# Kernel tuning notes

Hardware: AMD Instinct MI355X
Metric: run time of the kernel (lower is better)

The kernel has to match this reference:

```python
import jax, jax.numpy as jnp
import numpy as np

B, N, R, L = 32768, 9, 128, 2
F = 4 * R  # ffn hidden
EPS = 1e-5


def setup_inputs() -> dict:
    key = jax.random.key(0)
    ks = jax.random.split(key, 12)
    graph = jax.random.uniform(ks[0], (B, N, N), dtype=jnp.float32)  # weighted adjacency
    op_idx = jax.random.randint(ks[1], (B, N), 0, 7)
    op_table = jax.random.normal(ks[2], (7, R), dtype=jnp.float32)
    dev_embed = jax.random.normal(ks[3], (1, R), dtype=jnp.float32)
    s = 1.0 / np.sqrt(R)
    gcn_W = jax.random.normal(ks[4], (L, R, R), dtype=jnp.float32) * s
    gcn_b = jnp.zeros((L, R), dtype=jnp.float32)
    ln_g = jnp.ones((L, R), dtype=jnp.float32)
    ln_b = jnp.zeros((L, R), dtype=jnp.float32)
    ffn_W1 = jax.random.normal(ks[5], (L, R, F), dtype=jnp.float32) * s
    ffn_b1 = jnp.zeros((L, F), dtype=jnp.float32)
    ffn_W2 = jax.random.normal(ks[6], (L, F, R), dtype=jnp.float32) * (1.0 / np.sqrt(F))
    ffn_b2 = jnp.zeros((L, R), dtype=jnp.float32)
    fc_w = jax.random.normal(ks[7], (R, 1), dtype=jnp.float32) * s
    fc_b = jnp.zeros((1,), dtype=jnp.float32)
    return dict(graph=graph, op_idx=op_idx, op_table=op_table, dev_embed=dev_embed,
                gcn_W=gcn_W, gcn_b=gcn_b, ln_g=ln_g, ln_b=ln_b,
                ffn_W1=ffn_W1, ffn_b1=ffn_b1, ffn_W2=ffn_W2, ffn_b2=ffn_b2,
                fc_w=fc_w, fc_b=fc_b)


def _layer_norm(x, g, b):
    mu = x.mean(-1, keepdims=True)
    var = ((x - mu) ** 2).mean(-1, keepdims=True)
    return (x - mu) * jax.lax.rsqrt(var + EPS) * g + b


def reference(graph, op_idx, op_table, dev_embed, gcn_W, gcn_b, ln_g, ln_b,
              ffn_W1, ffn_b1, ffn_W2, ffn_b2, fc_w, fc_b):
    # embedding lookup + broadcast-add of device embedding: [B, N, R]
    x = op_table[op_idx].reshape(B * N, R) + dev_embed
    x = x.reshape(B, N, R)
    # symmetric GCN normalization with self loops on the 9x9 adjacency
    a_hat = graph + jnp.eye(N, dtype=graph.dtype)[None]
    d_is = jax.lax.rsqrt(a_hat.sum(-1))  # [B, N]
    norm_adj = a_hat * d_is[:, :, None] * d_is[:, None, :]  # [B, N, N]
    for l in range(L):
        # message passing + linear
        h = jnp.einsum('bij,bjr->bir', norm_adj, x) @ gcn_W[l] + gcn_b[l]
        h = jax.nn.relu(h)
        h = _layer_norm(h, ln_g[l], ln_b[l])
        # residual FFN
        h = h + jax.nn.relu(h @ ffn_W1[l] + ffn_b1[l]) @ ffn_W2[l] + ffn_b2[l]
        x = h
    pooled = x.mean(axis=1)  # [B, R] readout over the 9 nodes
    y = jax.nn.sigmoid(pooled @ fc_w + fc_b).squeeze(-1)  # [B]
    return y
```

## Files before the change

### kernel.cpp

```cpp
#include <hip/hip_runtime.h>
#include <math.h>

#define NN 9
#define RR 128
#define FF 512
#define LL 2
#define GPB 7
#define ROWS 63

typedef __attribute__((ext_vector_type(8))) short bf16x8;
typedef __attribute__((ext_vector_type(4))) float f32x4;

__device__ __forceinline__ float4 ld4(const float* p) { return *reinterpret_cast<const float4*>(p); }
__device__ __forceinline__ float2 ld2(const float* p) { return *reinterpret_cast<const float2*>(p); }
__device__ __forceinline__ void st4(float* p, const float4 v) { *reinterpret_cast<float4*>(p) = v; }

__device__ __forceinline__ ushort f2bf(float f) {
    unsigned u = __float_as_uint(f);
    return (ushort)((u + 0x7fffu + ((u >> 16) & 1u)) >> 16);
}
__device__ __forceinline__ float bf2f(ushort h) { return __uint_as_float(((unsigned)h) << 16); }

__device__ __forceinline__ void async16(void* lds, const void* g) {
    __builtin_amdgcn_global_load_lds(
        (const __attribute__((address_space(1))) unsigned int*)g,
        (__attribute__((address_space(3))) unsigned int*)lds,
        16, 0, 0);
}

#define SWZ(row, c) ((row) * 128 + ((c) ^ (((row) & 7) << 3)))

__global__ __launch_bounds__(256)
void pack_weights(const float* __restrict__ gcn_W,
                  const float* __restrict__ ffn_W1,
                  const float* __restrict__ ffn_W2,
                  ushort* __restrict__ wsw)
{
    const int t    = blockIdx.x * 256 + threadIdx.x;
    const int lane = t & 63;
    const int slot = t >> 6;
    const int grp  = lane >> 4, cl = lane & 15;

    const float* src; int ldn, kbase, n;
    if (slot < 64) {
        const int l = slot >> 5, ks = (slot >> 3) & 3, nt = slot & 7;
        src = gcn_W + l * RR * RR; ldn = RR;
        kbase = ks * 32 + grp * 8;
        n = nt * 16 + cl;
    } else if (slot < 320) {
        const int s = slot - 64;
        const int l = s >> 7, p = (s >> 5) & 3, ks = (s >> 3) & 3, nt = s & 7;
        src = ffn_W1 + l * RR * FF; ldn = FF;
        kbase = ks * 32 + grp * 8;
        n = p * 128 + nt * 16 + cl;
    } else {
        const int s = slot - 320;
        const int l = s >> 7, p = (s >> 5) & 3, ks = (s >> 3) & 3, nt = s & 7;
        src = ffn_W2 + l * FF * RR; ldn = RR;
        kbase = p * 128 + ks * 32 + grp * 8;
        n = nt * 16 + cl;
    }
    ushort v[8];
    #pragma unroll
    for (int j = 0; j < 8; ++j) v[j] = f2bf(src[(size_t)(kbase + j) * ldn + n]);
    uint4 o;
    o.x = v[0] | ((unsigned)v[1] << 16);
    o.y = v[2] | ((unsigned)v[3] << 16);
    o.z = v[4] | ((unsigned)v[5] << 16);
    o.w = v[6] | ((unsigned)v[7] << 16);
    *reinterpret_cast<uint4*>(wsw + ((size_t)slot * 64 + lane) * 8) = o;
}

__device__ __forceinline__ int g16(int l, int kh)         { return (l * 4 + kh * 2) * 8; }
__device__ __forceinline__ int w1g(int l, int p, int kh)  { return 64 + ((l * 4 + p) * 4 + kh * 2) * 8; }
__device__ __forceinline__ int w2g(int l, int p, int kh)  { return 320 + ((l * 4 + p) * 4 + kh * 2) * 8; }

#define MMA_GROUP2(T, APTR0, APTR1, BUFSEL)                                    \
    {                                                                          \
        const unsigned char* bb_ = &wbuf[BUFSEL][lane << 4];                   \
        const bf16x8 af0_ = *(const bf16x8*)(APTR0);                           \
        _Pragma("unroll")                                                      \
        for (int nt = 0; nt < 8; ++nt)                                         \
            T[nt] = __builtin_amdgcn_mfma_f32_16x16x32_bf16(                   \
                af0_, *(const bf16x8*)(bb_ + (nt << 10)), T[nt], 0, 0, 0);     \
        const bf16x8 af1_ = *(const bf16x8*)(APTR1);                           \
        _Pragma("unroll")                                                      \
        for (int nt = 0; nt < 8; ++nt)                                         \
            T[nt] = __builtin_amdgcn_mfma_f32_16x16x32_bf16(                   \
                af1_, *(const bf16x8*)(bb_ + ((8 + nt) << 10)), T[nt], 0, 0, 0); \
    }

#define STAGE16(DST, FRAGBASE)                                                 \
    {                                                                          \
        const unsigned char* g_ = wsb + ((size_t)((FRAGBASE) + ms * 4) << 10)  \
                                      + (lane << 4);                           \
        async16(&wbuf[DST][(ms * 4 + 0) << 10], g_);                           \
        async16(&wbuf[DST][(ms * 4 + 1) << 10], g_ + 1024);                    \
        async16(&wbuf[DST][(ms * 4 + 2) << 10], g_ + 2048);                    \
        async16(&wbuf[DST][(ms * 4 + 3) << 10], g_ + 3072);                    \
    }

__global__ __launch_bounds__(256, 2)
void backbone_mfma(const float* __restrict__ graph,
                   const int*   __restrict__ op_idx,
                   const float* __restrict__ op_table,
                   const float* __restrict__ dev_embed,
                   const float* __restrict__ gcn_b,
                   const float* __restrict__ ln_g,
                   const float* __restrict__ ln_b,
                   const float* __restrict__ ffn_b1,
                   const float* __restrict__ ffn_b2,
                   const float* __restrict__ fc_w,
                   const float* __restrict__ fc_b,
                   const ushort* __restrict__ wsw,
                   float* __restrict__ out,
                   const int nB)
{
    __shared__ alignas(16) ushort sA[64 * 128];
    __shared__ alignas(16) ushort sGH[64 * 128];
    __shared__ float sNA[GPB][81];
    __shared__ float sD[ROWS];
    __shared__ float sRD[64];
    __shared__ alignas(16) unsigned char wbuf[2][16384];

    const int tid  = threadIdx.x;
    const int lane = tid & 63;
    const int ms   = tid >> 6;
    const int grp  = lane >> 4;
    const int cl   = lane & 15;
    const int c0   = lane * 2;
    const int R0   = ms * 16;
    const int b0   = blockIdx.x * GPB;

    const unsigned char* wsb = (const unsigned char*)wsw;

    if (tid < 64) {
        *reinterpret_cast<unsigned*>(&sA[SWZ(63, tid * 2)])  = 0u;
        *reinterpret_cast<unsigned*>(&sGH[SWZ(63, tid * 2)]) = 0u;
    }

    {
        const float2 dv = ld2(&dev_embed[c0]);
        #pragma unroll
        for (int rr = 0; rr < 16; ++rr) {
            const int row = R0 + rr;
            if (row < ROWS) {
                const int gi = row / NN, ni = row - gi * NN;
                const int gg = min(b0 + gi, nB - 1);
                const int idx = op_idx[gg * NN + ni];
                float2 v = ld2(&op_table[idx * RR + c0]);
                unsigned pk = f2bf(v.x + dv.x) | ((unsigned)f2bf(v.y + dv.y) << 16);
                *reinterpret_cast<unsigned*>(&sA[SWZ(row, c0)]) = pk;
            }
        }
    }

    for (int e = tid; e < GPB * 81; e += 256) {
        const int gi = e / 81, r = e - gi * 81;
        const int i = r / NN, j = r - i * NN;
        const int gg = min(b0 + gi, nB - 1);
        sNA[gi][r] = graph[(size_t)gg * 81 + r] + (i == j ? 1.0f : 0.0f);
    }
    __syncthreads();
    if (tid < ROWS) {
        const int gi = tid / NN, i = tid - gi * NN;
        float s = 0.f;
        #pragma unroll
        for (int j = 0; j < NN; ++j) s += sNA[gi][i * NN + j];
        sD[tid] = rsqrtf(s);
    }
    __syncthreads();
    for (int e = tid; e < GPB * 81; e += 256) {
        const int gi = e / 81, r = e - gi * 81;
        const int i = r / NN, j = r - i * NN;
        sNA[gi][r] *= sD[gi * NN + i] * sD[gi * NN + j];
    }

    int cur = 0;
    STAGE16(0, g16(0, 0));
    __syncthreads();

    f32x4 acc[8];

    for (int l = 0; l < LL; ++l) {
        {
            const int g0 = R0 / NN, g1 = (R0 + 15) / NN;
            for (int gi = g0; gi <= g1 && gi < GPB; ++gi) {
                float xr[2 * NN];
                #pragma unroll
                for (int j = 0; j < NN; ++j) {
                    unsigned u = *reinterpret_cast<const unsigned*>(&sA[SWZ(gi * NN + j, c0)]);
                    xr[2 * j]     = bf2f((ushort)(u & 0xffffu));
                    xr[2 * j + 1] = bf2f((ushort)(u >> 16));
                }
                const int rlo = max(R0, gi * NN), rhi = min(R0 + 16, gi * NN + NN);
                for (int row = rlo; row < rhi; ++row) {
                    const int ni = row - gi * NN;
                    float a0 = 0.f, a1 = 0.f;
                    #pragma unroll
                    for (int j = 0; j < NN; ++j) {
                        const float w = sNA[gi][ni * NN + j];
                        a0 = fmaf(w, xr[2 * j], a0);
                        a1 = fmaf(w, xr[2 * j + 1], a1);
                    }
                    unsigned pk = f2bf(a0) | ((unsigned)f2bf(a1) << 16);
                    *reinterpret_cast<unsigned*>(&sGH[SWZ(row, c0)]) = pk;
                }
            }
        }

        #pragma unroll
        for (int nt = 0; nt < 8; ++nt) acc[nt] = (f32x4){0.f, 0.f, 0.f, 0.f};
        #pragma unroll
        for (int kh = 0; kh < 2; ++kh) {
            const int nb = (kh == 0) ? g16(l, 1) : w1g(l, 0, 0);
            STAGE16(cur ^ 1, nb);
            MMA_GROUP2(acc,
                       &sGH[SWZ(R0 + cl, (kh * 2 + 0) * 32 + grp * 8)],
                       &sGH[SWZ(R0 + cl, (kh * 2 + 1) * 32 + grp * 8)], cur);
            __syncthreads();
            cur ^= 1;
        }

        {
            float sv[4] = {0.f, 0.f, 0.f, 0.f}, qv[4] = {0.f, 0.f, 0.f, 0.f};
            #pragma unroll
            for (int nt = 0; nt < 8; ++nt) {
                const float gb = gcn_b[l * RR + nt * 16 + cl];
                #pragma unroll
                for (int r = 0; r < 4; ++r) {
                    float v = fmaxf(acc[nt][r] + gb, 0.f);
                    acc[nt][r] = v;
                    sv[r] += v; qv[r] += v * v;
                }
            }
            #pragma unroll
            for (int r = 0; r < 4; ++r) {
                #pragma unroll
                for (int m = 1; m <= 8; m <<= 1) {
                    sv[r] += __shfl_xor(sv[r], m);
                    qv[r] += __shfl_xor(qv[r], m);
                }
            }
            float mu[4], rs[4];
            #pragma unroll
            for (int r = 0; r < 4; ++r) {
                mu[r] = sv[r] * (1.f / RR);
                const float var = qv[r] * (1.f / RR) - mu[r] * mu[r];
                rs[r] = rsqrtf(var + 1e-5f);
            }
            #pragma unroll
            for (int nt = 0; nt < 8; ++nt) {
                const float lgv = ln_g[l * RR + nt * 16 + cl];
                const float lbv = ln_b[l * RR + nt * 16 + cl];
                #pragma unroll
                for (int r = 0; r < 4; ++r)
                    acc[nt][r] = (acc[nt][r] - mu[r]) * rs[r] * lgv + lbv;
            }
        }

        #pragma unroll
        for (int nt = 0; nt < 8; ++nt) {
            #pragma unroll
            for (int r = 0; r < 4; ++r)
                sA[SWZ(R0 + grp * 4 + r, nt * 16 + cl)] = f2bf(acc[nt][r]);
        }
        #pragma unroll
        for (int nt = 0; nt < 8; ++nt) {
            const float b2v = ffn_b2[l * RR + nt * 16 + cl];
            #pragma unroll
            for (int r = 0; r < 4; ++r) acc[nt][r] += b2v;
        }

        for (int p = 0; p < 4; ++p) {
            f32x4 t[8];
            #pragma unroll
            for (int nt = 0; nt < 8; ++nt) {
                const float b1v = ffn_b1[l * FF + p * 128 + nt * 16 + cl];
                t[nt] = (f32x4){b1v, b1v, b1v, b1v};
            }
            #pragma unroll
            for (int kh = 0; kh < 2; ++kh) {
                const int nb = (kh == 0) ? w1g(l, p, 1) : w2g(l, p, 0);
                STAGE16(cur ^ 1, nb);
                MMA_GROUP2(t,
                           &sA[SWZ(R0 + cl, (kh * 2 + 0) * 32 + grp * 8)],
                           &sA[SWZ(R0 + cl, (kh * 2 + 1) * 32 + grp * 8)], cur);
                __syncthreads();
                cur ^= 1;
            }
            #pragma unroll
            for (int nt = 0; nt < 8; ++nt) {
                #pragma unroll
                for (int r = 0; r < 4; ++r)
                    sGH[SWZ(R0 + grp * 4 + r, nt * 16 + cl)] = f2bf(fmaxf(t[nt][r], 0.f));
            }
            #pragma unroll
            for (int kh = 0; kh < 2; ++kh) {
                const bool last = (l == LL - 1) && (p == 3) && (kh == 1);
                const int nb = (kh == 0) ? w2g(l, p, 1)
                             : ((p < 3) ? w1g(l, p + 1, 0) : g16(l + 1, 0));
                if (!last) STAGE16(cur ^ 1, nb);
                MMA_GROUP2(acc,
                           &sGH[SWZ(R0 + cl, (kh * 2 + 0) * 32 + grp * 8)],
                           &sGH[SWZ(R0 + cl, (kh * 2 + 1) * 32 + grp * 8)], cur);
                __syncthreads();
                cur ^= 1;
            }
        }

        if (l + 1 < LL) {
            #pragma unroll
            for (int nt = 0; nt < 8; ++nt) {
                #pragma unroll
                for (int r = 0; r < 4; ++r)
                    sA[SWZ(R0 + grp * 4 + r, nt * 16 + cl)] = f2bf(acc[nt][r]);
            }
            __syncthreads();
        }
    }

    {
        float p4[4] = {0.f, 0.f, 0.f, 0.f};
        #pragma unroll
        for (int nt = 0; nt < 8; ++nt) {
            const float fw = fc_w[nt * 16 + cl];
            #pragma unroll
            for (int r = 0; r < 4; ++r) p4[r] = fmaf(acc[nt][r], fw, p4[r]);
        }
        #pragma unroll
        for (int r = 0; r < 4; ++r) {
            #pragma unroll
            for (int m = 1; m <= 8; m <<= 1) p4[r] += __shfl_xor(p4[r], m);
        }
        if (cl == 0) {
            #pragma unroll
            for (int r = 0; r < 4; ++r) sRD[R0 + grp * 4 + r] = p4[r];
        }
        __syncthreads();
        if (tid < GPB) {
            const int g = b0 + tid;
            if (g < nB) {
                float s = 0.f;
                #pragma unroll
                for (int n = 0; n < NN; ++n) s += sRD[tid * NN + n];
                out[g] = 1.f / (1.f + expf(-(s * (1.f / 9.f) + fc_b[0])));
            }
        }
    }
}

__device__ __forceinline__ void fma4(float4& d, const float a, const float4 w) {
    d.x = fmaf(a, w.x, d.x); d.y = fmaf(a, w.y, d.y);
    d.z = fmaf(a, w.z, d.z); d.w = fmaf(a, w.w, d.w);
}
__device__ __forceinline__ void xadd32(float4& v) {
    v.x += __shfl_xor(v.x, 32); v.y += __shfl_xor(v.y, 32);
    v.z += __shfl_xor(v.z, 32); v.w += __shfl_xor(v.w, 32);
}
__device__ __forceinline__ void relu4f(float4& v) {
    v.x = fmaxf(v.x, 0.f); v.y = fmaxf(v.y, 0.f);
    v.z = fmaxf(v.z, 0.f); v.w = fmaxf(v.w, 0.f);
}

__global__ __launch_bounds__(256)
void backbone_fp32(const float* __restrict__ graph, const int* __restrict__ op_idx,
                   const float* __restrict__ op_table, const float* __restrict__ dev_embed,
                   const float* __restrict__ gcn_W, const float* __restrict__ gcn_b,
                   const float* __restrict__ ln_g, const float* __restrict__ ln_b,
                   const float* __restrict__ ffn_W1, const float* __restrict__ ffn_b1,
                   const float* __restrict__ ffn_W2, const float* __restrict__ ffn_b2,
                   const float* __restrict__ fc_w, const float* __restrict__ fc_b,
                   float* __restrict__ out)
{
    __shared__ float sX[4][NN][RR];
    __shared__ float sT[4][NN][RR];
    __shared__ float sNA[4][81];
    __shared__ float sD[4][NN];

    const int tid  = threadIdx.x;
    const int lane = tid & 63;
    const int cg   = tid & 31;
    const int half = (tid >> 5) & 1;
    const int ms   = tid >> 6;
    const int c0   = cg * 4;
    const int k0   = half * 64;
    const int g    = blockIdx.x * 4 + ms;

    {
        const float dv0 = dev_embed[lane];
        const float dv1 = dev_embed[lane + 64];
        #pragma unroll
        for (int j = 0; j < NN; ++j) {
            const int idx = op_idx[g * NN + j];
            sX[ms][j][lane]      = op_table[idx * RR + lane]      + dv0;
            sX[ms][j][lane + 64] = op_table[idx * RR + lane + 64] + dv1;
        }
    }
    {
        const float* gp = graph + (size_t)g * 81;
        { const int i = lane / NN, j = lane - i * NN;
          sNA[ms][lane] = gp[lane] + (i == j ? 1.0f : 0.0f); }
        if (lane < 17) { const int e = lane + 64; const int i = e / NN, j = e - i * NN;
          sNA[ms][e] = gp[e] + (i == j ? 1.0f : 0.0f); }
        if (lane < NN) {
            float s = 0.f;
            #pragma unroll
            for (int j = 0; j < NN; ++j) s += sNA[ms][lane * NN + j];
            sD[ms][lane] = rsqrtf(s);
        }
        { const int i = lane / NN, j = lane - i * NN; sNA[ms][lane] *= sD[ms][i] * sD[ms][j]; }
        if (lane < 17) { const int e = lane + 64; const int i = e / NN, j = e - i * NN;
          sNA[ms][e] *= sD[ms][i] * sD[ms][j]; }
    }

    float4 acc[NN];
    for (int l = 0; l < LL; ++l) {
        const float* gw = gcn_W  + l * RR * RR;
        const float* gb = gcn_b  + l * RR;
        const float* lg = ln_g   + l * RR;
        const float* lb = ln_b   + l * RR;
        const float* w1 = ffn_W1 + l * RR * FF;
        const float* b1 = ffn_b1 + l * FF;
        const float* w2 = ffn_W2 + l * FF * RR;
        const float* b2 = ffn_b2 + l * RR;
        {
            float4 xv[NN];
            #pragma unroll
            for (int j = 0; j < NN; ++j) xv[j] = ld4(&sX[ms][j][c0]);
            #pragma unroll
            for (int ii = 0; ii < 5; ++ii) {
                const int i = ii + half * 5;
                if (i < NN) {
                    float4 a = make_float4(0.f, 0.f, 0.f, 0.f);
                    #pragma unroll
                    for (int j = 0; j < NN; ++j) fma4(a, sNA[ms][i * NN + j], xv[j]);
                    st4(&sT[ms][i][c0], a);
                }
            }
        }
        float4 h[NN];
        {
            const float4 z4 = make_float4(0.f, 0.f, 0.f, 0.f);
            const float4 gbv = ld4(&gb[c0]);
            const float4 ini = half ? z4 : gbv;
            #pragma unroll
            for (int i = 0; i < NN; ++i) h[i] = ini;
            #pragma unroll 2
            for (int kk = 0; kk < 64; kk += 4) {
                const float* wp = gw + (size_t)(k0 + kk) * RR + c0;
                const float4 wv0 = ld4(wp), wv1 = ld4(wp + RR), wv2 = ld4(wp + 2 * RR), wv3 = ld4(wp + 3 * RR);
                #pragma unroll
                for (int i = 0; i < NN; ++i) {
                    const float4 a = ld4(&sT[ms][i][k0 + kk]);
                    fma4(h[i], a.x, wv0); fma4(h[i], a.y, wv1);
                    fma4(h[i], a.z, wv2); fma4(h[i], a.w, wv3);
                }
            }
            #pragma unroll
            for (int i = 0; i < NN; ++i) xadd32(h[i]);
        }
        {
            const float4 lgv = ld4(&lg[c0]);
            const float4 lbv = ld4(&lb[c0]);
            #pragma unroll
            for (int i = 0; i < NN; ++i) {
                float4 v = h[i]; relu4f(v);
                float s = v.x + v.y + v.z + v.w;
                float q = v.x*v.x + v.y*v.y + v.z*v.z + v.w*v.w;
                #pragma unroll
                for (int m = 1; m <= 16; m <<= 1) { s += __shfl_xor(s, m); q += __shfl_xor(q, m); }
                const float mu = s * (1.f / RR);
                const float var = q * (1.f / RR) - mu * mu;
                const float rs = rsqrtf(var + 1e-5f);
                v.x = (v.x - mu) * rs * lgv.x + lbv.x;
                v.y = (v.y - mu) * rs * lgv.y + lbv.y;
                v.z = (v.z - mu) * rs * lgv.z + lbv.z;
                v.w = (v.w - mu) * rs * lgv.w + lbv.w;
                h[i] = v;
            }
        }
        #pragma unroll
        for (int i = 0; i < NN; ++i) st4(&sX[ms][i][c0], h[i]);
        {
            const float4 b2v = ld4(&b2[c0]);
            #pragma unroll
            for (int i = 0; i < NN; ++i) {
                if (half) acc[i] = make_float4(0.f, 0.f, 0.f, 0.f);
                else { acc[i] = h[i];
                       acc[i].x += b2v.x; acc[i].y += b2v.y; acc[i].z += b2v.z; acc[i].w += b2v.w; }
            }
        }
        for (int p = 0; p < 4; ++p) {
            const int f0 = p * RR + c0;
            float4 t[NN];
            {
                const float4 z4 = make_float4(0.f, 0.f, 0.f, 0.f);
                const float4 b1v = ld4(&b1[f0]);
                const float4 ini = half ? z4 : b1v;
                #pragma unroll
                for (int i = 0; i < NN; ++i) t[i] = ini;
            }
            #pragma unroll 2
            for (int kk = 0; kk < 64; kk += 4) {
                const float* wp = w1 + (size_t)(k0 + kk) * FF + f0;
                const float4 wv0 = ld4(wp), wv1 = ld4(wp + FF), wv2 = ld4(wp + 2 * FF), wv3 = ld4(wp + 3 * FF);
                #pragma unroll
                for (int i = 0; i < NN; ++i) {
                    const float4 a = ld4(&sX[ms][i][k0 + kk]);
                    fma4(t[i], a.x, wv0); fma4(t[i], a.y, wv1);
                    fma4(t[i], a.z, wv2); fma4(t[i], a.w, wv3);
                }
            }
            #pragma unroll
            for (int i = 0; i < NN; ++i) { xadd32(t[i]); relu4f(t[i]); st4(&sT[ms][i][c0], t[i]); }
            #pragma unroll 2
            for (int kk = 0; kk < 64; kk += 4) {
                const float* wp = w2 + (size_t)(p * RR + k0 + kk) * RR + c0;
                const float4 wv0 = ld4(wp), wv1 = ld4(wp + RR), wv2 = ld4(wp + 2 * RR), wv3 = ld4(wp + 3 * RR);
                #pragma unroll
                for (int i = 0; i < NN; ++i) {
                    const float4 a = ld4(&sT[ms][i][k0 + kk]);
                    fma4(acc[i], a.x, wv0); fma4(acc[i], a.y, wv1);
                    fma4(acc[i], a.z, wv2); fma4(acc[i], a.w, wv3);
                }
            }
        }
        #pragma unroll
        for (int i = 0; i < NN; ++i) xadd32(acc[i]);
        if (l + 1 < LL) {
            #pragma unroll
            for (int i = 0; i < NN; ++i) st4(&sX[ms][i][c0], acc[i]);
        }
    }
    {
        const float4 fw = ld4(&fc_w[c0]);
        float4 pv = make_float4(0.f, 0.f, 0.f, 0.f);
        #pragma unroll
        for (int i = 0; i < NN; ++i) { pv.x += acc[i].x; pv.y += acc[i].y; pv.z += acc[i].z; pv.w += acc[i].w; }
        float part = (pv.x*fw.x + pv.y*fw.y + pv.z*fw.z + pv.w*fw.w) * (1.f / 9.f);
        #pragma unroll
        for (int m = 1; m <= 16; m <<= 1) part += __shfl_xor(part, m);
        if (lane == 0) out[g] = 1.f / (1.f + expf(-(part + fc_b[0])));
    }
}

extern "C" void kernel_launch(void* const* d_in, const int* in_sizes, int n_in,
                              void* d_out, int out_size, void* d_ws, size_t ws_size,
                              hipStream_t stream) {
    const float* graph     = (const float*)d_in[0];
    const int*   op_idx    = (const int*)  d_in[1];
    const float* op_table  = (const float*)d_in[2];
    const float* dev_embed = (const float*)d_in[3];
    const float* gcn_W     = (const float*)d_in[4];
    const float* gcn_b     = (const float*)d_in[5];
    const float* ln_g      = (const float*)d_in[6];
    const float* ln_b      = (const float*)d_in[7];
    const float* ffn_W1    = (const float*)d_in[8];
    const float* ffn_b1    = (const float*)d_in[9];
    const float* ffn_W2    = (const float*)d_in[10];
    const float* ffn_b2    = (const float*)d_in[11];
    const float* fc_w      = (const float*)d_in[12];
    const float* fc_b      = (const float*)d_in[13];
    float* out = (float*)d_out;

    const int nB = in_sizes[0] / 81;
    const size_t WS_NEED = 576 * 1024;

    if (d_ws != nullptr && ws_size >= WS_NEED) {
        pack_weights<<<dim3(144), dim3(256), 0, stream>>>(gcn_W, ffn_W1, ffn_W2, (ushort*)d_ws);
        backbone_mfma<<<dim3((nB + GPB - 1) / GPB), dim3(256), 0, stream>>>(
            graph, op_idx, op_table, dev_embed, gcn_b, ln_g, ln_b,
            ffn_b1, ffn_b2, fc_w, fc_b, (const ushort*)d_ws, out, nB);
    } else {
        backbone_fp32<<<dim3(nB / 4), dim3(256), 0, stream>>>(
            graph, op_idx, op_table, dev_embed, gcn_W, gcn_b, ln_g, ln_b,
            ffn_W1, ffn_b1, ffn_W2, ffn_b2, fc_w, fc_b, out);
    }
}
```

Before: 384.7 us.

## Retile MFMA work per wave into 32-row by 64-column blocks

Result: no change. 389.7 us (+1.3%).

```diff
diff --git a/kernel.cpp b/kernel.cpp
--- a/kernel.cpp
+++ b/kernel.cpp
@@ -75,19 +75,23 @@
 __device__ __forceinline__ int w1g(int l, int p, int kh)  { return 64 + ((l * 4 + p) * 4 + kh * 2) * 8; }
 __device__ __forceinline__ int w2g(int l, int p, int kh)  { return 320 + ((l * 4 + p) * 4 + kh * 2) * 8; }
 
-#define MMA_GROUP2(T, APTR0, APTR1, BUFSEL)                                    \
+#define MMA22(T, SRCARR, KH, BUFSEL)                                           \
     {                                                                          \
         const unsigned char* bb_ = &wbuf[BUFSEL][lane << 4];                   \
-        const bf16x8 af0_ = *(const bf16x8*)(APTR0);                           \
         _Pragma("unroll")                                                      \
-        for (int nt = 0; nt < 8; ++nt)                                         \
-            T[nt] = __builtin_amdgcn_mfma_f32_16x16x32_bf16(                   \
-                af0_, *(const bf16x8*)(bb_ + (nt << 10)), T[nt], 0, 0, 0);     \
-        const bf16x8 af1_ = *(const bf16x8*)(APTR1);                           \
-        _Pragma("unroll")                                                      \
-        for (int nt = 0; nt < 8; ++nt)                                         \
-            T[nt] = __builtin_amdgcn_mfma_f32_16x16x32_bf16(                   \
-                af1_, *(const bf16x8*)(bb_ + ((8 + nt) << 10)), T[nt], 0, 0, 0); \
+        for (int ki = 0; ki < 2; ++ki) {                                       \
+            const bf16x8 a0_ = *(const bf16x8*)&SRCARR[SWZ(rh32 + cl,          \
+                                        ((KH) * 2 + ki) * 32 + grp * 8)];      \
+            const bf16x8 a1_ = *(const bf16x8*)&SRCARR[SWZ(rh32 + 16 + cl,     \
+                                        ((KH) * 2 + ki) * 32 + grp * 8)];      \
+            _Pragma("unroll")                                                  \
+            for (int nt = 0; nt < 4; ++nt) {                                   \
+                const bf16x8 b_ = *(const bf16x8*)(bb_ +                       \
+                                        ((ki * 8 + ch4 + nt) << 10));          \
+                T[nt]     = __builtin_amdgcn_mfma_f32_16x16x32_bf16(a0_, b_, T[nt], 0, 0, 0);     \
+                T[4 + nt] = __builtin_amdgcn_mfma_f32_16x16x32_bf16(a1_, b_, T[4 + nt], 0, 0, 0); \
+            }                                                                  \
+        }                                                                      \
     }
 
 #define STAGE16(DST, FRAGBASE)                                                 \
@@ -120,7 +124,8 @@
     __shared__ alignas(16) ushort sGH[64 * 128];
     __shared__ float sNA[GPB][81];
     __shared__ float sD[ROWS];
-    __shared__ float sRD[64];
+    __shared__ float2 sLN[64][2];
+    __shared__ float sRD[64][2];
     __shared__ alignas(16) unsigned char wbuf[2][16384];
 
     const int tid  = threadIdx.x;
@@ -129,6 +134,9 @@
     const int grp  = lane >> 4;
     const int cl   = lane & 15;
     const int c0   = lane * 2;
+    const int rh32 = (ms >> 1) * 32;
+    const int ch4  = (ms & 1) * 4;
+    const int cb   = ch4 * 16;
     const int R0   = ms * 16;
     const int b0   = blockIdx.x * GPB;
 
@@ -208,102 +216,129 @@
                 }
             }
         }
-
-        #pragma unroll
-        for (int nt = 0; nt < 8; ++nt) acc[nt] = (f32x4){0.f, 0.f, 0.f, 0.f};
+        __syncthreads();
+
+        #pragma unroll
+        for (int i = 0; i < 8; ++i) acc[i] = (f32x4){0.f, 0.f, 0.f, 0.f};
         #pragma unroll
         for (int kh = 0; kh < 2; ++kh) {
             const int nb = (kh == 0) ? g16(l, 1) : w1g(l, 0, 0);
             STAGE16(cur ^ 1, nb);
-            MMA_GROUP2(acc,
-                       &sGH[SWZ(R0 + cl, (kh * 2 + 0) * 32 + grp * 8)],
-                       &sGH[SWZ(R0 + cl, (kh * 2 + 1) * 32 + grp * 8)], cur);
+            MMA22(acc, sGH, kh, cur);
             __syncthreads();
             cur ^= 1;
         }
 
         {
-            float sv[4] = {0.f, 0.f, 0.f, 0.f}, qv[4] = {0.f, 0.f, 0.f, 0.f};
-            #pragma unroll
-            for (int nt = 0; nt < 8; ++nt) {
-                const float gb = gcn_b[l * RR + nt * 16 + cl];
+            float sv[8] = {0,0,0,0,0,0,0,0}, qv[8] = {0,0,0,0,0,0,0,0};
+            #pragma unroll
+            for (int rg = 0; rg < 2; ++rg) {
+                #pragma unroll
+                for (int nt = 0; nt < 4; ++nt) {
+                    const float gb = gcn_b[l * RR + cb + nt * 16 + cl];
+                    #pragma unroll
+                    for (int r = 0; r < 4; ++r) {
+                        float v = fmaxf(acc[rg * 4 + nt][r] + gb, 0.f);
+                        acc[rg * 4 + nt][r] = v;
+                        sv[rg * 4 + r] += v; qv[rg * 4 + r] += v * v;
+                    }
+                }
+            }
+            #pragma unroll
+            for (int i = 0; i < 8; ++i) {
+                #pragma unroll
+                for (int m = 1; m <= 8; m <<= 1) {
+                    sv[i] += __shfl_xor(sv[i], m);
+                    qv[i] += __shfl_xor(qv[i], m);
+                }
+            }
+            if (cl == 0) {
+                #pragma unroll
+                for (int rg = 0; rg < 2; ++rg)
+                    #pragma unroll
+                    for (int r = 0; r < 4; ++r)
+                        sLN[rh32 + rg * 16 + grp * 4 + r][ms & 1] =
+                            make_float2(sv[rg * 4 + r], qv[rg * 4 + r]);
+            }
+            __syncthreads();
+            float mu[8], rs[8];
+            #pragma unroll
+            for (int rg = 0; rg < 2; ++rg) {
                 #pragma unroll
                 for (int r = 0; r < 4; ++r) {
-                    float v = fmaxf(acc[nt][r] + gb, 0.f);
-                    acc[nt][r] = v;
-                    sv[r] += v; qv[r] += v * v;
-                }
-            }
-            #pragma unroll
-            for (int r = 0; r < 4; ++r) {
-                #pragma unroll
-                for (int m = 1; m <= 8; m <<= 1) {
-                    sv[r] += __shfl_xor(sv[r], m);
-                    qv[r] += __shfl_xor(qv[r], m);
-                }
-            }
-            float mu[4], rs[4];
-            #pragma unroll
-            for (int r = 0; r < 4; ++r) {
-                mu[r] = sv[r] * (1.f / RR);
-                const float var = qv[r] * (1.f / RR) - mu[r] * mu[r];
-                rs[r] = rsqrtf(var + 1e-5f);
-            }
-            #pragma unroll
-            for (int nt = 0; nt < 8; ++nt) {
-                const float lgv = ln_g[l * RR + nt * 16 + cl];
-                const float lbv = ln_b[l * RR + nt * 16 + cl];
+                    const float2 a = sLN[rh32 + rg * 16 + grp * 4 + r][0];
+                    const float2 b = sLN[rh32 + rg * 16 + grp * 4 + r][1];
+                    const float s = a.x + b.x, q = a.y + b.y;
+                    const float m_ = s * (1.f / RR);
+                    mu[rg * 4 + r] = m_;
+                    rs[rg * 4 + r] = rsqrtf(q * (1.f / RR) - m_ * m_ + 1e-5f);
+                }
+            }
+            #pragma unroll
+            for (int rg = 0; rg < 2; ++rg) {
+                #pragma unroll
+                for (int nt = 0; nt < 4; ++nt) {
+                    const float lgv = ln_g[l * RR + cb + nt * 16 + cl];
+                    const float lbv = ln_b[l * RR + cb + nt * 16 + cl];
+                    #pragma unroll
+                    for (int r = 0; r < 4; ++r)
+                        acc[rg * 4 + nt][r] = (acc[rg * 4 + nt][r] - mu[rg * 4 + r])
+                                              * rs[rg * 4 + r] * lgv + lbv;
+                }
+            }
+        }
+
+        #pragma unroll
+        for (int rg = 0; rg < 2; ++rg)
+            #pragma unroll
+            for (int nt = 0; nt < 4; ++nt)
                 #pragma unroll
                 for (int r = 0; r < 4; ++r)
-                    acc[nt][r] = (acc[nt][r] - mu[r]) * rs[r] * lgv + lbv;
-            }
-        }
-
-        #pragma unroll
-        for (int nt = 0; nt < 8; ++nt) {
-            #pragma unroll
-            for (int r = 0; r < 4; ++r)
-                sA[SWZ(R0 + grp * 4 + r, nt * 16 + cl)] = f2bf(acc[nt][r]);
-        }
-        #pragma unroll
-        for (int nt = 0; nt < 8; ++nt) {
-            const float b2v = ffn_b2[l * RR + nt * 16 + cl];
-            #pragma unroll
-            for (int r = 0; r < 4; ++r) acc[nt][r] += b2v;
-        }
+                    sA[SWZ(rh32 + rg * 16 + grp * 4 + r, cb + nt * 16 + cl)]
+                        = f2bf(acc[rg * 4 + nt][r]);
+        #pragma unroll
+        for (int rg = 0; rg < 2; ++rg)
+            #pragma unroll
+            for (int nt = 0; nt < 4; ++nt) {
+                const float b2v = ffn_b2[l * RR + cb + nt * 16 + cl];
+                #pragma unroll
+                for (int r = 0; r < 4; ++r) acc[rg * 4 + nt][r] += b2v;
+            }
+        __syncthreads();
 
         for (int p = 0; p < 4; ++p) {
             f32x4 t[8];
             #pragma unroll
-            for (int nt = 0; nt < 8; ++nt) {
-                const float b1v = ffn_b1[l * FF + p * 128 + nt * 16 + cl];
-                t[nt] = (f32x4){b1v, b1v, b1v, b1v};
-            }
+            for (int rg = 0; rg < 2; ++rg)
+                #pragma unroll
+                for (int nt = 0; nt < 4; ++nt) {
+                    const float b1v = ffn_b1[l * FF + p * 128 + cb + nt * 16 + cl];
+                    t[rg * 4 + nt] = (f32x4){b1v, b1v, b1v, b1v};
+                }
             #pragma unroll
             for (int kh = 0; kh < 2; ++kh) {
                 const int nb = (kh == 0) ? w1g(l, p, 1) : w2g(l, p, 0);
                 STAGE16(cur ^ 1, nb);
-                MMA_GROUP2(t,
-                           &sA[SWZ(R0 + cl, (kh * 2 + 0) * 32 + grp * 8)],
-                           &sA[SWZ(R0 + cl, (kh * 2 + 1) * 32 + grp * 8)], cur);
+                MMA22(t, sA, kh, cur);
                 __syncthreads();
                 cur ^= 1;
             }
             #pragma unroll
-            for (int nt = 0; nt < 8; ++nt) {
-                #pragma unroll
-                for (int r = 0; r < 4; ++r)
-                    sGH[SWZ(R0 + grp * 4 + r, nt * 16 + cl)] = f2bf(fmaxf(t[nt][r], 0.f));
-            }
+            for (int rg = 0; rg < 2; ++rg)
+                #pragma unroll
+                for (int nt = 0; nt < 4; ++nt)
+                    #pragma unroll
+                    for (int r = 0; r < 4; ++r)
+                        sGH[SWZ(rh32 + rg * 16 + grp * 4 + r, cb + nt * 16 + cl)]
+                            = f2bf(fmaxf(t[rg * 4 + nt][r], 0.f));
+            __syncthreads();
             #pragma unroll
             for (int kh = 0; kh < 2; ++kh) {
                 const bool last = (l == LL - 1) && (p == 3) && (kh == 1);
                 const int nb = (kh == 0) ? w2g(l, p, 1)
                              : ((p < 3) ? w1g(l, p + 1, 0) : g16(l + 1, 0));
                 if (!last) STAGE16(cur ^ 1, nb);
-                MMA_GROUP2(acc,
-                           &sGH[SWZ(R0 + cl, (kh * 2 + 0) * 32 + grp * 8)],
-                           &sGH[SWZ(R0 + cl, (kh * 2 + 1) * 32 + grp * 8)], cur);
+                MMA22(acc, sGH, kh, cur);
                 __syncthreads();
                 cur ^= 1;
             }
@@ -311,31 +346,39 @@
 
         if (l + 1 < LL) {
             #pragma unroll
-            for (int nt = 0; nt < 8; ++nt) {
+            for (int rg = 0; rg < 2; ++rg)
+                #pragma unroll
+                for (int nt = 0; nt < 4; ++nt)
+                    #pragma unroll
+                    for (int r = 0; r < 4; ++r)
+                        sA[SWZ(rh32 + rg * 16 + grp * 4 + r, cb + nt * 16 + cl)]
+                            = f2bf(acc[rg * 4 + nt][r]);
+            __syncthreads();
+        }
+    }
+
+    {
+        float p4[8] = {0,0,0,0,0,0,0,0};
+        #pragma unroll
+        for (int rg = 0; rg < 2; ++rg)
+            #pragma unroll
+            for (int nt = 0; nt < 4; ++nt) {
+                const float fw = fc_w[cb + nt * 16 + cl];
                 #pragma unroll
                 for (int r = 0; r < 4; ++r)
-                    sA[SWZ(R0 + grp * 4 + r, nt * 16 + cl)] = f2bf(acc[nt][r]);
-            }
-            __syncthreads();
-        }
-    }
-
-    {
-        float p4[4] = {0.f, 0.f, 0.f, 0.f};
-        #pragma unroll
-        for (int nt = 0; nt < 8; ++nt) {
-            const float fw = fc_w[nt * 16 + cl];
-            #pragma unroll
-            for (int r = 0; r < 4; ++r) p4[r] = fmaf(acc[nt][r], fw, p4[r]);
-        }
-        #pragma unroll
-        for (int r = 0; r < 4; ++r) {
-            #pragma unroll
-            for (int m = 1; m <= 8; m <<= 1) p4[r] += __shfl_xor(p4[r], m);
+                    p4[rg * 4 + r] = fmaf(acc[rg * 4 + nt][r], fw, p4[rg * 4 + r]);
+            }
+        #pragma unroll
+        for (int i = 0; i < 8; ++i) {
+            #pragma unroll
+            for (int m = 1; m <= 8; m <<= 1) p4[i] += __shfl_xor(p4[i], m);
         }
         if (cl == 0) {
             #pragma unroll
-            for (int r = 0; r < 4; ++r) sRD[R0 + grp * 4 + r] = p4[r];
+            for (int rg = 0; rg < 2; ++rg)
+                #pragma unroll
+                for (int r = 0; r < 4; ++r)
+                    sRD[rh32 + rg * 16 + grp * 4 + r][ms & 1] = p4[rg * 4 + r];
         }
         __syncthreads();
         if (tid < GPB) {
@@ -343,7 +386,8 @@
             if (g < nB) {
                 float s = 0.f;
                 #pragma unroll
-                for (int n = 0; n < NN; ++n) s += sRD[tid * NN + n];
+                for (int n = 0; n < NN; ++n)
+                    s += sRD[tid * NN + n][0] + sRD[tid * NN + n][1];
                 out[g] = 1.f / (1.f + expf(-(s * (1.f / 9.f) + fc_b[0])));
             }
         }
```
